# Kernel tuning notes

Hardware: AMD Instinct MI355X
Metric: run time of the kernel (lower is better)

The kernel has to match this reference:

```python
import jax, jax.numpy as jnp
import numpy as np

EPS = 1e-8  # torch CosineSimilarity eps


def setup_inputs() -> dict:
    key = jax.random.key(0)
    k1, k2, k3, k4 = jax.random.split(key, 4)
    N, m, D = 4096, 4, 256
    log_hazard = jax.random.normal(k1, (N,), dtype=jnp.float32)
    encoded_blocks = jax.random.normal(k2, (m, N, D), dtype=jnp.float32)
    time = jax.random.uniform(k3, (N,), dtype=jnp.float32, minval=0.01, maxval=10.0)
    event = jax.random.randint(k4, (N,), 0, 2).astype(jnp.int32)
    M = jnp.asarray(0.1, dtype=jnp.float32)
    return {"log_hazard": log_hazard, "encoded_blocks": encoded_blocks,
            "time": time, "event": event, "M": M}


def _cox_loss(log_hazard, time, event):
    # risk[i, j] = 1 if t_j >= t_i  (equivalent to (outer(t,t) >= t^2).T for t > 0)
    risk = (time[None, :] >= time[:, None]).astype(log_hazard.dtype)
    ev = event.astype(log_hazard.dtype)
    log_risk = jnp.log(risk @ jnp.exp(log_hazard))  # [N]
    return -jnp.sum(ev * (log_hazard - log_risk)) / jnp.sum(ev)


def _similarity_loss(encoded_blocks, M):
    # encoded_blocks: [m, N, D]
    m, N, D = encoded_blocks.shape
    norms = jnp.maximum(jnp.linalg.norm(encoded_blocks, axis=-1, keepdims=True), EPS)
    xn = encoded_blocks / norms                         # normalized embeddings [m,N,D]
    S = jnp.einsum('mid,mjd->mij', xn, xn)              # pairwise cosine sims [m,N,N]
    # modality is 'missing' for a patient if all features equal the first feature
    missing = jnp.all(encoded_blocks == encoded_blocks[..., :1], axis=-1)  # [m,N]
    valid = (~missing[:, :, None] & ~missing[:, None, :]).astype(S.dtype)  # [m,N,N]
    self_sim = jnp.diagonal(S, axis1=1, axis2=2)        # cos(x_i, x_i) per modality [m,N]
    psim = jnp.sum(valid * self_sim[:, :, None], axis=0)  # [N,N] patient self-similarity
    msim = jnp.sum(valid * S, axis=0)                     # [N,N] matched similarity
    offdiag = 1.0 - jnp.eye(N, dtype=S.dtype)
    return jnp.sum(offdiag * jax.nn.relu(M - msim + psim))


def reference(log_hazard, encoded_blocks, time, event, M):
    cox = _cox_loss(log_hazard, time, event)
    sim = _similarity_loss(encoded_blocks, M)
    return cox + sim
```

## Files before the change

kernel.cpp:

```cpp
#include <hip/hip_runtime.h>

#define N_PAT 4096
#define NMOD  4
#define OFFPAIRS 16773120.0

__global__ __launch_bounds__(256) void prep_cox_kernel(
    const float* __restrict__ eb, const float* __restrict__ h,
    const float* __restrict__ t,
    float* __restrict__ part_v, float* __restrict__ part_D,
    float* __restrict__ part_n, float* __restrict__ sumexp)
{
  __shared__ float shmem[8192];
  int tid = threadIdx.x;
  int wid = tid >> 6, lane = tid & 63;
  int b = blockIdx.x;

  if (b < 1024) {
    float* xsh = shmem;
    float* dsh = shmem + 1024;
    float* nsh = shmem + 1028;
    float4 acc = {0.f, 0.f, 0.f, 0.f};
    float Dacc = 0.f, nacc = 0.f;
#pragma unroll
    for (int rr = 0; rr < 4; ++rr) {
      int row = b * 16 + wid * 4 + rr;
      const float* base = eb + (size_t)row * 256;
      float4 v = *(const float4*)(base + lane * 4);
      float x0 = base[0];
      int eq = (v.x == x0) & (v.y == x0) & (v.z == x0) & (v.w == x0);
      float ss = v.x * v.x + v.y * v.y + v.z * v.z + v.w * v.w;
#pragma unroll
      for (int o = 32; o; o >>= 1) ss += __shfl_xor(ss, o, 64);
      int missing = __all(eq);
      float denom = fmaxf(sqrtf(ss), 1e-8f);
      float inv = missing ? 0.0f : (1.0f / denom);
      acc.x += v.x * inv; acc.y += v.y * inv;
      acc.z += v.z * inv; acc.w += v.w * inv;
      Dacc += missing ? 0.0f : (ss * inv * inv);
      nacc += missing ? 0.0f : 1.0f;
    }
    xsh[wid * 256 + lane * 4 + 0] = acc.x;
    xsh[wid * 256 + lane * 4 + 1] = acc.y;
    xsh[wid * 256 + lane * 4 + 2] = acc.z;
    xsh[wid * 256 + lane * 4 + 3] = acc.w;
    if (lane == 0) { dsh[wid] = Dacc; nsh[wid] = nacc; }
    __syncthreads();
    part_v[(size_t)b * 256 + tid] =
        (xsh[tid] + xsh[256 + tid]) + (xsh[512 + tid] + xsh[768 + tid]);
    if (tid == 0) part_D[b] = (dsh[0] + dsh[1]) + (dsh[2] + dsh[3]);
    if (tid == 1) part_n[b] = (nsh[0] + nsh[1]) + (nsh[2] + nsh[3]);
  } else {
    float* tl = shmem;
    float* el = shmem + 4096;
    for (int q = tid; q < N_PAT; q += 256) {
      tl[q] = t[q];
      el[q] = expf(h[q]);
    }
    __syncthreads();
    int cb = b - 1024;
#pragma unroll
    for (int r = 0; r < 4; ++r) {
      int i = cb * 16 + wid * 4 + r;
      float ti = tl[i];
      float s = 0.f;
#pragma unroll
      for (int it = 0; it < 16; ++it) {
        int j = (it * 64 + lane) * 4;
        float4 tv = *(const float4*)(&tl[j]);
        float4 ev = *(const float4*)(&el[j]);
        s += (tv.x >= ti) ? ev.x : 0.f;
        s += (tv.y >= ti) ? ev.y : 0.f;
        s += (tv.z >= ti) ? ev.z : 0.f;
        s += (tv.w >= ti) ? ev.w : 0.f;
      }
#pragma unroll
      for (int o = 32; o; o >>= 1) s += __shfl_xor(s, o, 64);
      if (lane == 0) sumexp[i] = s;
    }
  }
}

__global__ __launch_bounds__(256) void reduce_kernel(
    const float* __restrict__ part_v, const float* __restrict__ part_D,
    const float* __restrict__ part_n, const float* __restrict__ h,
    const int* __restrict__ ev, const float* __restrict__ sumexp,
    float* __restrict__ vsq_part, float* __restrict__ D_part,
    float* __restrict__ n_part, float* __restrict__ num_part,
    float* __restrict__ den_part)
{
  __shared__ float vsh[4][64];
  __shared__ float rsh[2][4];
  int tid = threadIdx.x, lane = tid & 63, wid = tid >> 6;
  int g = blockIdx.x;
  int m = g >> 2, dq = g & 3;

  int d = dq * 64 + lane;
  const float* vb = part_v + ((size_t)(m * 256 + wid * 64)) * 256 + d;
  float s = 0.f;
#pragma unroll 8
  for (int r = 0; r < 64; ++r) s += vb[(size_t)r * 256];
  vsh[wid][lane] = s;

  int i = g * 256 + tid;
  float e = (float)ev[i];
  float num = e * (h[i] - logf(sumexp[i]));
  float den = e;
#pragma unroll
  for (int o = 32; o; o >>= 1) {
    num += __shfl_xor(num, o, 64);
    den += __shfl_xor(den, o, 64);
  }
  if (lane == 0) { rsh[0][wid] = num; rsh[1][wid] = den; }
  __syncthreads();

  if (wid == 0) {
    float vd = (vsh[0][lane] + vsh[1][lane]) + (vsh[2][lane] + vsh[3][lane]);
    float vsq = vd * vd;
#pragma unroll
    for (int o = 32; o; o >>= 1) vsq += __shfl_xor(vsq, o, 64);
    float Dv = part_D[g * 64 + lane];
    float nv = part_n[g * 64 + lane];
#pragma unroll
    for (int o = 32; o; o >>= 1) {
      Dv += __shfl_xor(Dv, o, 64);
      nv += __shfl_xor(nv, o, 64);
    }
    if (lane == 0) {
      vsq_part[g] = vsq;
      D_part[g]   = Dv;
      n_part[g]   = nv;
      num_part[g] = rsh[0][0] + rsh[0][1] + rsh[0][2] + rsh[0][3];
      den_part[g] = rsh[1][0] + rsh[1][1] + rsh[1][2] + rsh[1][3];
    }
  }
}

__global__ __launch_bounds__(64) void finalize_kernel(
    const float* __restrict__ vsq_part, const float* __restrict__ D_part,
    const float* __restrict__ n_part, const float* __restrict__ num_part,
    const float* __restrict__ den_part, const float* __restrict__ Mp,
    float* __restrict__ out)
{
  if (threadIdx.x == 0) {
    double sim = (double)Mp[0] * OFFPAIRS;
    for (int m = 0; m < NMOD; ++m) {
      double Dm = 0.0, nm = 0.0;
      for (int q = 0; q < 4; ++q) {
        Dm += (double)D_part[m * 4 + q];
        nm += (double)n_part[m * 4 + q];
      }
      sim += nm * Dm;
    }
    for (int g = 0; g < 16; ++g) sim -= (double)vsq_part[g];
    double n = 0.0, d = 0.0;
    for (int g = 0; g < 16; ++g) { n += (double)num_part[g]; d += (double)den_part[g]; }
    out[0] = (float)(-n / d + sim);
  }
}

extern "C" void kernel_launch(void* const* d_in, const int* in_sizes, int n_in,
                              void* d_out, int out_size, void* d_ws, size_t ws_size,
                              hipStream_t stream)
{
  const float* h  = (const float*)d_in[0];
  const float* eb = (const float*)d_in[1];
  const float* tm = (const float*)d_in[2];
  const int*   ev = (const int*)d_in[3];
  const float* Mp = (const float*)d_in[4];
  float* out = (float*)d_out;

  char* ws = (char*)d_ws;
  float* part_v   = (float*)ws;
  float* part_D   = part_v + 1024 * 256;
  float* part_n   = part_D + 1024;
  float* sumexp   = part_n + 1024;
  float* vsq_part = sumexp + N_PAT;
  float* D_part   = vsq_part + 16;
  float* n_part   = D_part + 16;
  float* num_part = n_part + 16;
  float* den_part = num_part + 16;

  prep_cox_kernel<<<dim3(1280), dim3(256), 0, stream>>>(
      eb, h, tm, part_v, part_D, part_n, sumexp);
  reduce_kernel<<<dim3(16), dim3(256), 0, stream>>>(
      part_v, part_D, part_n, h, ev, sumexp,
      vsq_part, D_part, n_part, num_part, den_part);
  finalize_kernel<<<dim3(1), dim3(64), 0, stream>>>(
      vsq_part, D_part, n_part, num_part, den_part, Mp, out);
}
```

Measured before the change: 18.91 us.

## Fuse finalize into reduce via last-block atomic counter, move Cox log-sum into prep

```diff
diff --git a/kernel.cpp b/kernel.cpp
--- a/kernel.cpp
+++ b/kernel.cpp
@@ -6,16 +6,19 @@
 
 __global__ __launch_bounds__(256) void prep_cox_kernel(
     const float* __restrict__ eb, const float* __restrict__ h,
-    const float* __restrict__ t,
+    const float* __restrict__ t, const int* __restrict__ ev,
     float* __restrict__ part_v, float* __restrict__ part_D,
-    float* __restrict__ part_n, float* __restrict__ sumexp)
+    float* __restrict__ part_n, float* __restrict__ num_part,
+    float* __restrict__ den_part, int* __restrict__ ctr)
 {
   __shared__ float shmem[8192];
+  __shared__ float rsh[8];
   int tid = threadIdx.x;
   int wid = tid >> 6, lane = tid & 63;
   int b = blockIdx.x;
 
   if (b < 1024) {
+    if (b == 0 && tid == 0) *ctr = 0;
     float* xsh = shmem;
     float* dsh = shmem + 1024;
     float* nsh = shmem + 1028;
@@ -58,6 +61,7 @@
     }
     __syncthreads();
     int cb = b - 1024;
+    float numw = 0.f, denw = 0.f;
 #pragma unroll
     for (int r = 0; r < 4; ++r) {
       int i = cb * 16 + wid * 4 + r;
@@ -67,29 +71,38 @@
       for (int it = 0; it < 16; ++it) {
         int j = (it * 64 + lane) * 4;
         float4 tv = *(const float4*)(&tl[j]);
-        float4 ev = *(const float4*)(&el[j]);
-        s += (tv.x >= ti) ? ev.x : 0.f;
-        s += (tv.y >= ti) ? ev.y : 0.f;
-        s += (tv.z >= ti) ? ev.z : 0.f;
-        s += (tv.w >= ti) ? ev.w : 0.f;
+        float4 evv = *(const float4*)(&el[j]);
+        s += (tv.x >= ti) ? evv.x : 0.f;
+        s += (tv.y >= ti) ? evv.y : 0.f;
+        s += (tv.z >= ti) ? evv.z : 0.f;
+        s += (tv.w >= ti) ? evv.w : 0.f;
       }
 #pragma unroll
       for (int o = 32; o; o >>= 1) s += __shfl_xor(s, o, 64);
-      if (lane == 0) sumexp[i] = s;
+      if (lane == 0) {
+        float e = (float)ev[i];
+        numw += e * (h[i] - logf(s));
+        denw += e;
+      }
     }
+    if (lane == 0) { rsh[wid] = numw; rsh[4 + wid] = denw; }
+    __syncthreads();
+    if (tid == 0) num_part[cb] = (rsh[0] + rsh[1]) + (rsh[2] + rsh[3]);
+    if (tid == 1) den_part[cb] = (rsh[4] + rsh[5]) + (rsh[6] + rsh[7]);
   }
 }
 
-__global__ __launch_bounds__(256) void reduce_kernel(
+__global__ __launch_bounds__(256) void reduce_finalize_kernel(
     const float* __restrict__ part_v, const float* __restrict__ part_D,
-    const float* __restrict__ part_n, const float* __restrict__ h,
-    const int* __restrict__ ev, const float* __restrict__ sumexp,
-    float* __restrict__ vsq_part, float* __restrict__ D_part,
-    float* __restrict__ n_part, float* __restrict__ num_part,
-    float* __restrict__ den_part)
+    const float* __restrict__ part_n, const float* __restrict__ num_part,
+    const float* __restrict__ den_part, const float* __restrict__ Mp,
+    float* __restrict__ vsq_part, float* __restrict__ D_part16,
+    float* __restrict__ n_part16, float* __restrict__ num16,
+    float* __restrict__ den16, int* __restrict__ ctr,
+    float* __restrict__ out)
 {
   __shared__ float vsh[4][64];
-  __shared__ float rsh[2][4];
+  __shared__ int lastflag;
   int tid = threadIdx.x, lane = tid & 63, wid = tid >> 6;
   int g = blockIdx.x;
   int m = g >> 2, dq = g & 3;
@@ -100,61 +113,55 @@
 #pragma unroll 8
   for (int r = 0; r < 64; ++r) s += vb[(size_t)r * 256];
   vsh[wid][lane] = s;
-
-  int i = g * 256 + tid;
-  float e = (float)ev[i];
-  float num = e * (h[i] - logf(sumexp[i]));
-  float den = e;
-#pragma unroll
-  for (int o = 32; o; o >>= 1) {
-    num += __shfl_xor(num, o, 64);
-    den += __shfl_xor(den, o, 64);
-  }
-  if (lane == 0) { rsh[0][wid] = num; rsh[1][wid] = den; }
   __syncthreads();
 
   if (wid == 0) {
     float vd = (vsh[0][lane] + vsh[1][lane]) + (vsh[2][lane] + vsh[3][lane]);
     float vsq = vd * vd;
-#pragma unroll
-    for (int o = 32; o; o >>= 1) vsq += __shfl_xor(vsq, o, 64);
     float Dv = part_D[g * 64 + lane];
     float nv = part_n[g * 64 + lane];
+    float nm = (lane < 16) ? num_part[g * 16 + lane] : 0.f;
+    float dn = (lane < 16) ? den_part[g * 16 + lane] : 0.f;
 #pragma unroll
     for (int o = 32; o; o >>= 1) {
-      Dv += __shfl_xor(Dv, o, 64);
-      nv += __shfl_xor(nv, o, 64);
+      vsq += __shfl_xor(vsq, o, 64);
+      Dv  += __shfl_xor(Dv, o, 64);
+      nv  += __shfl_xor(nv, o, 64);
+      nm  += __shfl_xor(nm, o, 64);
+      dn  += __shfl_xor(dn, o, 64);
     }
     if (lane == 0) {
       vsq_part[g] = vsq;
-      D_part[g]   = Dv;
-      n_part[g]   = nv;
-      num_part[g] = rsh[0][0] + rsh[0][1] + rsh[0][2] + rsh[0][3];
-      den_part[g] = rsh[1][0] + rsh[1][1] + rsh[1][2] + rsh[1][3];
+      D_part16[g] = Dv;
+      n_part16[g] = nv;
+      num16[g]    = nm;
+      den16[g]    = dn;
     }
   }
-}
+  __syncthreads();
+  if (tid == 0) {
+    __threadfence();
+    int prev = __hip_atomic_fetch_add(ctr, 1, __ATOMIC_ACQ_REL,
+                                      __HIP_MEMORY_SCOPE_AGENT);
+    lastflag = (prev == 15);
+  }
+  __syncthreads();
 
-__global__ __launch_bounds__(64) void finalize_kernel(
-    const float* __restrict__ vsq_part, const float* __restrict__ D_part,
-    const float* __restrict__ n_part, const float* __restrict__ num_part,
-    const float* __restrict__ den_part, const float* __restrict__ Mp,
-    float* __restrict__ out)
-{
-  if (threadIdx.x == 0) {
+  if (lastflag && tid == 0) {
+    __threadfence();
     double sim = (double)Mp[0] * OFFPAIRS;
-    for (int m = 0; m < NMOD; ++m) {
-      double Dm = 0.0, nm = 0.0;
+    for (int mm = 0; mm < NMOD; ++mm) {
+      double Dm = 0.0, nmm = 0.0;
       for (int q = 0; q < 4; ++q) {
-        Dm += (double)D_part[m * 4 + q];
-        nm += (double)n_part[m * 4 + q];
+        Dm  += (double)D_part16[mm * 4 + q];
+        nmm += (double)n_part16[mm * 4 + q];
       }
-      sim += nm * Dm;
+      sim += nmm * Dm;
     }
-    for (int g = 0; g < 16; ++g) sim -= (double)vsq_part[g];
-    double n = 0.0, d = 0.0;
-    for (int g = 0; g < 16; ++g) { n += (double)num_part[g]; d += (double)den_part[g]; }
-    out[0] = (float)(-n / d + sim);
+    for (int q = 0; q < 16; ++q) sim -= (double)vsq_part[q];
+    double n = 0.0, dd = 0.0;
+    for (int q = 0; q < 16; ++q) { n += (double)num16[q]; dd += (double)den16[q]; }
+    out[0] = (float)(-n / dd + sim);
   }
 }
 
@@ -173,18 +180,18 @@
   float* part_v   = (float*)ws;
   float* part_D   = part_v + 1024 * 256;
   float* part_n   = part_D + 1024;
-  float* sumexp   = part_n + 1024;
-  float* vsq_part = sumexp + N_PAT;
-  float* D_part   = vsq_part + 16;
-  float* n_part   = D_part + 16;
-  float* num_part = n_part + 16;
-  float* den_part = num_part + 16;
+  float* num_part = part_n + 1024;
+  float* den_part = num_part + 256;
+  float* vsq_part = den_part + 256;
+  float* D_part16 = vsq_part + 16;
+  float* n_part16 = D_part16 + 16;
+  float* num16    = n_part16 + 16;
+  float* den16    = num16 + 16;
+  int*   ctr      = (int*)(den16 + 16);
 
   prep_cox_kernel<<<dim3(1280), dim3(256), 0, stream>>>(
-      eb, h, tm, part_v, part_D, part_n, sumexp);
-  reduce_kernel<<<dim3(16), dim3(256), 0, stream>>>(
-      part_v, part_D, part_n, h, ev, sumexp,
-      vsq_part, D_part, n_part, num_part, den_part);
-  finalize_kernel<<<dim3(1), dim3(64), 0, stream>>>(
-      vsq_part, D_part, n_part, num_part, den_part, Mp, out);
+      eb, h, tm, ev, part_v, part_D, part_n, num_part, den_part, ctr);
+  reduce_finalize_kernel<<<dim3(16), dim3(256), 0, stream>>>(
+      part_v, part_D, part_n, num_part, den_part, Mp,
+      vsq_part, D_part16, n_part16, num16, den16, ctr, out);
 }
```

After: 19.61 us. 3.7% more time.
